# Kernel tuning notes

Measured on AMD Instinct MI355X. Metric: run time of the kernel, lower is better.

Reference implementation:

```python
import jax, jax.numpy as jnp
import numpy as np

VOCAB = 50257
BATCH = 512
SEQ = 1024


def setup_inputs() -> dict:
    key = jax.random.key(0)
    kx, kidf = jax.random.split(key)
    x = jax.random.randint(kx, (BATCH, SEQ), 0, VOCAB, dtype=jnp.int64)
    # idf weights are positive; uniform in (0.1, 5.0) mimics real idf values
    idf = jax.random.uniform(kidf, (VOCAB,), dtype=jnp.float32, minval=0.1, maxval=5.0)
    return {"x": x, "idf": idf}


def reference(x, idf):
    B, S = x.shape
    V = idf.shape[0]
    # term-frequency histogram: scatter-add directly into (B, V) accumulator,
    # equivalent to the one-hot scatter_ + sum over seq in the original
    rows = jnp.arange(B, dtype=x.dtype)[:, None]           # (B, 1)
    tf = jnp.zeros((B, V), dtype=jnp.float32).at[rows, x].add(1.0)
    tfidf = tf * idf                                        # (B, V)
    n = jnp.sum(tfidf, axis=1, keepdims=True)               # (B, 1)
    return tfidf / n
```

## Files before the change

kernel.cpp:

```cpp
#include <hip/hip_runtime.h>


constexpr int VOCAB = 50257;
constexpr int SEQ = 1024;
constexpr int BATCH = 512;
constexpr int NT = 1024;

__global__ __launch_bounds__(NT)
void tfidf_kernel(const int* __restrict__ x,
                  const float* __restrict__ idf,
                  float* __restrict__ out) {
    __shared__ float red[NT / 64];
    __shared__ float s_inv_n;

    const int b   = blockIdx.x;
    const int tid = threadIdx.x;

    const int   tok    = x[(size_t)b * SEQ + tid];
    const float my_idf = idf[tok];

    float* __restrict__ orow = out + (size_t)b * VOCAB;

    const int head = (4 - (b & 3)) & 3;
    const int n4   = (VOCAB - head) >> 2;
    const int tail = VOCAB - head - (n4 << 2);

    if (tid < head) orow[tid] = 0.0f;
    float4* __restrict__ p4 = (float4*)(orow + head);
    const float4 z4 = make_float4(0.0f, 0.0f, 0.0f, 0.0f);
    for (int c = tid; c < n4; c += NT) p4[c] = z4;
    if (tid < tail) orow[head + (n4 << 2) + tid] = 0.0f;

    float v = my_idf;
    #pragma unroll
    for (int off = 32; off > 0; off >>= 1) v += __shfl_down(v, off, 64);
    if ((tid & 63) == 0) red[tid >> 6] = v;
    __syncthreads();
    if (tid == 0) {
        float n = 0.0f;
        #pragma unroll
        for (int w = 0; w < NT / 64; ++w) n += red[w];
        s_inv_n = 1.0f / n;
    }
    __syncthreads();

    atomicAdd(orow + tok, my_idf * s_inv_n);
}

extern "C" void kernel_launch(void* const* d_in, const int* in_sizes, int n_in,
                              void* d_out, int out_size, void* d_ws, size_t ws_size,
                              hipStream_t stream) {
    const int*   x   = (const int*)d_in[0];
    const float* idf = (const float*)d_in[1];
    float*       out = (float*)d_out;
    tfidf_kernel<<<dim3(BATCH), dim3(NT), 0, stream>>>(x, idf, out);
}
```

Before: 128.1 us.

## Build histogram in shared memory per vocab segment and stream rows out

Splits each batch row into four vocab segments, one block each, and accumulates the normalized tf-idf histogram in LDS with shared atomics. Each segment is then written to global memory once with float4 stores, replacing the earlier pattern of zeroing the row globally and then doing global atomics. Every block re-reads the full row of tokens and idf values to compute the normalizer, which repeats that reduction four times. The segment buffer uses about 50KB of LDS, which limits how many blocks can be resident per CU.

```diff
diff --git a/kernel.cpp b/kernel.cpp
--- a/kernel.cpp
+++ b/kernel.cpp
@@ -1,50 +1,67 @@
 #include <hip/hip_runtime.h>
 
 
-constexpr int VOCAB = 50257;
-constexpr int SEQ = 1024;
-constexpr int BATCH = 512;
-constexpr int NT = 1024;
+constexpr int VOCAB  = 50257;
+constexpr int SEQ    = 1024;
+constexpr int BATCH  = 512;
+constexpr int NSEG   = 4;
+constexpr int SEGLEN = (VOCAB + NSEG - 1) / NSEG;
+constexpr int NT     = 256;
 
 __global__ __launch_bounds__(NT)
 void tfidf_kernel(const int* __restrict__ x,
                   const float* __restrict__ idf,
                   float* __restrict__ out) {
+    __shared__ float seg[SEGLEN];
     __shared__ float red[NT / 64];
-    __shared__ float s_inv_n;
 
-    const int b   = blockIdx.x;
+    const int blk = blockIdx.x;
+    const int b   = blk >> 2;
+    const int s   = blk & 3;
     const int tid = threadIdx.x;
 
-    const int   tok    = x[(size_t)b * SEQ + tid];
-    const float my_idf = idf[tok];
+    const int lo  = s * SEGLEN;
+    const int len = (SEGLEN < VOCAB - lo) ? SEGLEN : (VOCAB - lo);
 
-    float* __restrict__ orow = out + (size_t)b * VOCAB;
+    const int4 t4 = ((const int4*)(x + (size_t)b * SEQ))[tid];
 
-    const int head = (4 - (b & 3)) & 3;
-    const int n4   = (VOCAB - head) >> 2;
-    const int tail = VOCAB - head - (n4 << 2);
+    {
+        float4* z = (float4*)seg;
+        const float4 z4 = make_float4(0.f, 0.f, 0.f, 0.f);
+        for (int c = tid; c < SEGLEN / 4; c += NT) z[c] = z4;
+        if (tid < SEGLEN - (SEGLEN / 4) * 4) seg[(SEGLEN / 4) * 4 + tid] = 0.f;
+    }
 
-    if (tid < head) orow[tid] = 0.0f;
-    float4* __restrict__ p4 = (float4*)(orow + head);
-    const float4 z4 = make_float4(0.0f, 0.0f, 0.0f, 0.0f);
-    for (int c = tid; c < n4; c += NT) p4[c] = z4;
-    if (tid < tail) orow[head + (n4 << 2) + tid] = 0.0f;
-
-    float v = my_idf;
+    const float i0 = idf[t4.x], i1 = idf[t4.y], i2 = idf[t4.z], i3 = idf[t4.w];
+    float v = (i0 + i1) + (i2 + i3);
     #pragma unroll
     for (int off = 32; off > 0; off >>= 1) v += __shfl_down(v, off, 64);
     if ((tid & 63) == 0) red[tid >> 6] = v;
     __syncthreads();
-    if (tid == 0) {
-        float n = 0.0f;
-        #pragma unroll
-        for (int w = 0; w < NT / 64; ++w) n += red[w];
-        s_inv_n = 1.0f / n;
-    }
+    const float inv_n = 1.0f / ((red[0] + red[1]) + (red[2] + red[3]));
+
+    if (t4.x >= lo && t4.x < lo + len) atomicAdd(&seg[t4.x - lo], i0 * inv_n);
+    if (t4.y >= lo && t4.y < lo + len) atomicAdd(&seg[t4.y - lo], i1 * inv_n);
+    if (t4.z >= lo && t4.z < lo + len) atomicAdd(&seg[t4.z - lo], i2 * inv_n);
+    if (t4.w >= lo && t4.w < lo + len) atomicAdd(&seg[t4.w - lo], i3 * inv_n);
     __syncthreads();
 
-    atomicAdd(orow + tok, my_idf * s_inv_n);
+    const size_t g0 = (size_t)b * VOCAB + lo;
+    float* __restrict__ o = out + g0;
+    const int head = (int)((4 - (g0 & 3)) & 3);
+    const int n4   = (len - head) >> 2;
+    const int tail = len - head - (n4 << 2);
+
+    if (tid < head) o[tid] = seg[tid];
+    float4* __restrict__ p4 = (float4*)(o + head);
+    for (int c = tid; c < n4; c += NT) {
+        const int i = head + (c << 2);
+        p4[c] = make_float4(seg[i], seg[i + 1], seg[i + 2], seg[i + 3]);
+    }
+    if (tid < tail) {
+        const int i = head + (n4 << 2) + tid;
+        o[i] = seg[i];
+    }
 }
 
 extern "C" void kernel_launch(void* const* d_in, const int* in_sizes, int n_in,
@@ -53,5 +70,5 @@
     const int*   x   = (const int*)d_in[0];
     const float* idf = (const float*)d_in[1];
     float*       out = (float*)d_out;
-    tfidf_kernel<<<dim3(BATCH), dim3(NT), 0, stream>>>(x, idf, out);
+    tfidf_kernel<<<dim3(BATCH * NSEG), dim3(NT), 0, stream>>>(x, idf, out);
 }
```

Result: faster. 114.2 us (-10.9%).

## Build per-row token histogram in shared memory and write output densely

Applied to the files above, without the earlier changes.

Replaces the zero-fill-then-global-atomicAdd scheme with a per-block histogram in LDS, packing two 16-bit counts per word. After the histogram and the normalization sum are done, each block writes its full output row in one pass as count*idf*inv_n using float4 stores. This removes the global atomics and their ordering against the zero-fill stores. In exchange, every block must read the whole idf vector (about 200KB, L2-cached across blocks) and uses about 100KB of LDS, which limits how many blocks fit on a CU.

```diff
diff --git a/kernel.cpp b/kernel.cpp
--- a/kernel.cpp
+++ b/kernel.cpp
@@ -1,50 +1,68 @@
 #include <hip/hip_runtime.h>
 
 
-constexpr int VOCAB = 50257;
-constexpr int SEQ = 1024;
-constexpr int BATCH = 512;
-constexpr int NT = 1024;
+constexpr int VOCAB   = 50257;
+constexpr int SEQ     = 1024;
+constexpr int BATCH   = 512;
+constexpr int HWORDS  = (VOCAB + 1) / 2;
+constexpr int HWORDS4 = ((HWORDS + 3) / 4) * 4;
+constexpr int NT      = 1024;
 
 __global__ __launch_bounds__(NT)
 void tfidf_kernel(const int* __restrict__ x,
                   const float* __restrict__ idf,
                   float* __restrict__ out) {
+    __shared__ __align__(16) unsigned int cnt[HWORDS4];
     __shared__ float red[NT / 64];
-    __shared__ float s_inv_n;
 
     const int b   = blockIdx.x;
     const int tid = threadIdx.x;
 
-    const int   tok    = x[(size_t)b * SEQ + tid];
+    const int tok = x[(size_t)b * SEQ + tid];
+
+    {
+        uint4* z = (uint4*)cnt;
+        const uint4 z4 = make_uint4(0u, 0u, 0u, 0u);
+        for (int i = tid; i < HWORDS4 / 4; i += NT) z[i] = z4;
+    }
+
     const float my_idf = idf[tok];
+    __syncthreads();
 
-    float* __restrict__ orow = out + (size_t)b * VOCAB;
-
-    const int head = (4 - (b & 3)) & 3;
-    const int n4   = (VOCAB - head) >> 2;
-    const int tail = VOCAB - head - (n4 << 2);
-
-    if (tid < head) orow[tid] = 0.0f;
-    float4* __restrict__ p4 = (float4*)(orow + head);
-    const float4 z4 = make_float4(0.0f, 0.0f, 0.0f, 0.0f);
-    for (int c = tid; c < n4; c += NT) p4[c] = z4;
-    if (tid < tail) orow[head + (n4 << 2) + tid] = 0.0f;
+    atomicAdd(&cnt[tok >> 1], (tok & 1) ? 65536u : 1u);
 
     float v = my_idf;
     #pragma unroll
     for (int off = 32; off > 0; off >>= 1) v += __shfl_down(v, off, 64);
     if ((tid & 63) == 0) red[tid >> 6] = v;
     __syncthreads();
-    if (tid == 0) {
-        float n = 0.0f;
-        #pragma unroll
-        for (int w = 0; w < NT / 64; ++w) n += red[w];
-        s_inv_n = 1.0f / n;
+    float nsum = 0.0f;
+    #pragma unroll
+    for (int w = 0; w < NT / 64; ++w) nsum += red[w];
+    const float inv_n = 1.0f / nsum;
+
+    float* __restrict__ orow = out + (size_t)b * VOCAB;
+    const int head = (4 - (b & 3)) & 3;
+    const int n4   = (VOCAB - head) >> 2;
+    const int tail = VOCAB - head - (n4 << 2);
+
+    auto elem = [&](int vi) -> float {
+        const unsigned w = cnt[vi >> 1];
+        const unsigned c = (vi & 1) ? (w >> 16) : (w & 0xffffu);
+        return (float)c * idf[vi] * inv_n;
+    };
+
+    if (tid < head) orow[tid] = elem(tid);
+    float4* __restrict__ p4 = (float4*)(orow + head);
+    #pragma unroll 4
+    for (int c = tid; c < n4; c += NT) {
+        const int i = head + (c << 2);
+        p4[c] = make_float4(elem(i), elem(i + 1), elem(i + 2), elem(i + 3));
     }
-    __syncthreads();
-
-    atomicAdd(orow + tok, my_idf * s_inv_n);
+    if (tid < tail) {
+        const int i = head + (n4 << 2) + tid;
+        orow[i] = elem(i);
+    }
 }
 
 extern "C" void kernel_launch(void* const* d_in, const int* in_sizes, int n_in,
```

Result: faster. 111.7 us (-12.8%).
